# Kernel tuning notes

Measured on AMD Instinct MI355X. Metric: run time of the kernel, lower is better.

The kernel has to match this reference:

```python
import jax, jax.numpy as jnp
import numpy as np

B, S, D, H = 4, 2048, 1024, 16
HD = D // H

def setup_inputs() -> dict:
    key = jax.random.key(0)
    ks = jax.random.split(key, 11)
    scale = 1.0 / np.sqrt(D)
    return {
        "query": jax.random.normal(ks[0], (B, S, D), jnp.float32),
        "key_": jax.random.normal(ks[1], (B, S, D), jnp.float32),
        "value": jax.random.normal(ks[2], (B, S, D), jnp.float32),
        "wq": jax.random.normal(ks[3], (D, D), jnp.float32) * scale,
        "bq": jnp.zeros((D,), jnp.float32),
        "wk": jax.random.normal(ks[4], (D, D), jnp.float32) * scale,
        "bk": jnp.zeros((D,), jnp.float32),
        "wv": jax.random.normal(ks[5], (D, D), jnp.float32) * scale,
        "bv": jnp.zeros((D,), jnp.float32),
        "wo": jax.random.normal(ks[6], (D, D), jnp.float32) * scale,
        "bo": jnp.zeros((D,), jnp.float32),
    }

def _split_heads(x):
    b, s, _ = x.shape
    return x.reshape(b, s, H, HD).transpose(0, 2, 1, 3)  # [B,H,S,HD]

def reference(query, key_, value, wq, bq, wk, bk, wv, bv, wo, bo):
    q = _split_heads(query @ wq + bq)
    k = _split_heads(key_ @ wk + bk)
    v = _split_heads(value @ wv + bv)
    scores = jnp.einsum('bhqd,bhkd->bhqk', q, k) / jnp.sqrt(jnp.float32(HD))
    attn = jax.nn.softmax(scores, axis=-1)
    ctx = jnp.einsum('bhqk,bhkd->bhqd', attn, v)
    ctx = ctx.transpose(0, 2, 1, 3).reshape(B, S, D)
    return ctx @ wo + bo
```

## Files before the change

### kernel.cpp

```cpp
#include <hip/hip_runtime.h>

typedef _Float16 f16;
typedef _Float16 f16x8 __attribute__((ext_vector_type(8)));
typedef _Float16 f16x4 __attribute__((ext_vector_type(4)));
typedef float    f32x4 __attribute__((ext_vector_type(4)));
typedef float    f32x16 __attribute__((ext_vector_type(16)));

#define MROWS 8192
#define KDIM  1024
#define SEQ   2048
#define HDIM  64
#define QKV_LD 3072

#if __has_builtin(__builtin_amdgcn_exp2f)
#define EXP2(x) __builtin_amdgcn_exp2f(x)
#else
#define EXP2(x) exp2f(x)
#endif

#define AS1 __attribute__((address_space(1)))
#define AS3 __attribute__((address_space(3)))

__device__ __forceinline__ int swz5(int row) { return (row ^ (row >> 3)) & 7; }

__global__ __launch_bounds__(256) void prep_k(const float* __restrict__ q_,
                                              const float* __restrict__ k_,
                                              const float* __restrict__ v_,
                                              const float* __restrict__ w0,
                                              const float* __restrict__ w1,
                                              const float* __restrict__ w2,
                                              const float* __restrict__ w3,
                                              const float* __restrict__ bq,
                                              const float* __restrict__ bk,
                                              const float* __restrict__ bv,
                                              f16* __restrict__ X16,
                                              f16* __restrict__ qkvT,
                                              f16* __restrict__ woT,
                                              float* __restrict__ b3) {
  __shared__ float t[32][33];
  const int bid = blockIdx.x;
  const int tid = threadIdx.x;
  if (bid < 24576) {
    int y = bid >> 13;
    int i = (bid & 8191) * 256 + tid;
    const float* src = (y == 0) ? q_ : (y == 1) ? k_ : v_;
    float4 v = ((const float4*)src)[i];
    f16x4 o = { (f16)v.x, (f16)v.y, (f16)v.z, (f16)v.w };
    *(f16x4*)&X16[(size_t)y * 8388608 + (size_t)i * 4] = o;
  } else if (bid < 28672) {
    int local = bid - 24576;
    int z  = local >> 10;
    int by = ((local >> 5) & 31) * 32;
    int bx = (local & 31) * 32;
    const float* w = (z == 0) ? w0 : (z == 1) ? w1 : (z == 2) ? w2 : w3;
    f16* wt = (z == 3) ? woT : (qkvT + z * 1048576);
    int tx = tid & 31, ty = tid >> 5;
    #pragma unroll
    for (int i = ty; i < 32; i += 8) t[i][tx] = w[(size_t)(by + i) * KDIM + bx + tx];
    __syncthreads();
    #pragma unroll
    for (int i = ty; i < 32; i += 8) wt[(size_t)(bx + i) * KDIM + by + tx] = (f16)t[tx][i];
  } else {
    int i = (bid - 28672) * 256 + tid;
    float v;
    if (i < 1024) v = bq[i]; else if (i < 2048) v = bk[i - 1024]; else v = bv[i - 2048];
    b3[i] = v;
  }
}

template<bool OUT_F16>
__global__ __launch_bounds__(256) void gemm_k(const f16* __restrict__ A0, size_t aStride,
                                              const f16* __restrict__ Bt,
                                              const float* __restrict__ bias,
                                              void* __restrict__ Cout, int ldc) {
  __shared__ f16 sA[128 * 64];
  __shared__ f16 sB[128 * 64];
  const int tid  = threadIdx.x;
  const int lane = tid & 63;
  const int r    = lane & 15;
  const int q    = lane >> 4;
  const int wave = tid >> 6;
  const int m0 = blockIdx.x * 128;
  const int ng = blockIdx.z * 1024 + blockIdx.y * 128;
  const int wm = (wave >> 1) * 64;
  const int wn = (wave & 1) * 64;
  const f16* A = A0 + (size_t)blockIdx.z * aStride;

  f32x4 acc[4][4];
  #pragma unroll
  for (int i = 0; i < 4; ++i)
    #pragma unroll
    for (int j = 0; j < 4; ++j) acc[i][j] = (f32x4){0.f, 0.f, 0.f, 0.f};

  for (int kt = 0; kt < KDIM; kt += 64) {
    #pragma unroll
    for (int issue = 0; issue < 4; ++issue) {
      int g   = issue * 256 + tid;
      int row = g >> 3;
      int csw = (g & 7) ^ (row & 7);
      const f16* gA = A  + (size_t)(m0 + row) * KDIM + kt + csw * 8;
      const f16* gB = Bt + (size_t)(ng + row) * KDIM + kt + csw * 8;
      int lb = __builtin_amdgcn_readfirstlane((issue * 256 + (tid & ~63)) * 16);
      __builtin_amdgcn_global_load_lds((const AS1 void*)gA,
                                       (AS3 void*)((char*)sA + lb), 16, 0, 0);
      __builtin_amdgcn_global_load_lds((const AS1 void*)gB,
                                       (AS3 void*)((char*)sB + lb), 16, 0, 0);
    }
    __syncthreads();
    #pragma unroll
    for (int kk = 0; kk < 64; kk += 32) {
      f16x8 af[4], bf[4];
      #pragma unroll
      for (int mi = 0; mi < 4; ++mi) {
        int row = wm + mi * 16 + r;
        int cs  = ((kk >> 3) + q) ^ (row & 7);
        af[mi] = *(const f16x8*)&sA[row * 64 + cs * 8];
      }
      #pragma unroll
      for (int ni = 0; ni < 4; ++ni) {
        int row = wn + ni * 16 + r;
        int cs  = ((kk >> 3) + q) ^ (row & 7);
        bf[ni] = *(const f16x8*)&sB[row * 64 + cs * 8];
      }
      #pragma unroll
      for (int mi = 0; mi < 4; ++mi)
        #pragma unroll
        for (int ni = 0; ni < 4; ++ni)
          acc[mi][ni] = __builtin_amdgcn_mfma_f32_16x16x32_f16(af[mi], bf[ni], acc[mi][ni], 0, 0, 0);
    }
    __syncthreads();
  }
  #pragma unroll
  for (int ni = 0; ni < 4; ++ni) {
    int col = ng + wn + ni * 16 + r;
    float bv = bias[col];
    #pragma unroll
    for (int mi = 0; mi < 4; ++mi) {
      int rowb = m0 + wm + mi * 16 + q * 4;
      #pragma unroll
      for (int reg = 0; reg < 4; ++reg) {
        float v = acc[mi][ni][reg] + bv;
        if constexpr (OUT_F16) ((f16*)Cout)[(size_t)(rowb + reg) * ldc + col] = (f16)v;
        else                   ((float*)Cout)[(size_t)(rowb + reg) * ldc + col] = v;
      }
    }
  }
}

__global__ __launch_bounds__(512, 2) void gemm256_k(const f16* __restrict__ A0,
                                                    const f16* __restrict__ Bt,
                                                    const float* __restrict__ bias,
                                                    f16* __restrict__ Cout) {
  __shared__ f16 smem[65536];
  const int tid  = threadIdx.x;
  const int lane = tid & 63;
  const int r    = lane & 15;
  const int q    = lane >> 4;
  const int wave = tid >> 6;
  const int wm   = wave >> 2;
  const int wn   = wave & 3;

  const int id  = blockIdx.x;
  const int swz = (id & 7) * 48 + (id >> 3);
  const int bx  = swz & 31;
  const int by  = swz >> 5;
  const int m0  = bx * 256;
  const int n0  = by * 256;
  const f16* A  = A0 + (size_t)(by >> 2) * 8388608;

  const int srow0 = tid >> 3;
  const int srow1 = (512 + tid) >> 3;
  const int sg0 = (tid & 7) ^ (srow0 & 7);
  const int sg1 = (tid & 7) ^ (srow1 & 7);
  const f16* gA0 = A  + (size_t)(m0 + srow0) * KDIM + sg0 * 8;
  const f16* gA1 = A  + (size_t)(m0 + srow1) * KDIM + sg1 * 8;
  const f16* gB0 = Bt + (size_t)(n0 + srow0) * KDIM + sg0 * 8;
  const f16* gB1 = Bt + (size_t)(n0 + srow1) * KDIM + sg1 * 8;
  const int lb0 = __builtin_amdgcn_readfirstlane((tid & ~63) * 16);
  const int lb1 = __builtin_amdgcn_readfirstlane((512 + (tid & ~63)) * 16);

  auto issueA = [&](int s, int hi) {
    char* base = (char*)smem + (s & 1) * 65536 + hi * 16384;
    const f16* s0 = gA0 + (size_t)hi * (128 * KDIM) + s * 64;
    const f16* s1 = gA1 + (size_t)hi * (128 * KDIM) + s * 64;
    __builtin_amdgcn_global_load_lds((const AS1 void*)s0, (AS3 void*)(base + lb0), 16, 0, 0);
    __builtin_amdgcn_global_load_lds((const AS1 void*)s1, (AS3 void*)(base + lb1), 16, 0, 0);
  };
  auto issueB = [&](int s, int hi) {
    char* base = (char*)smem + (s & 1) * 65536 + 32768 + hi * 16384;
    const f16* s0 = gB0 + (size_t)hi * (128 * KDIM) + s * 64;
    const f16* s1 = gB1 + (size_t)hi * (128 * KDIM) + s * 64;
    __builtin_amdgcn_global_load_lds((const AS1 void*)s0, (AS3 void*)(base + lb0), 16, 0, 0);
    __builtin_amdgcn_global_load_lds((const AS1 void*)s1, (AS3 void*)(base + lb1), 16, 0, 0);
  };

  auto readA = [&](int s, int qa, f16x8 (&af)[4][2]) {
    const f16* rg = smem + (s & 1) * 32768 + qa * 8192;
    #pragma unroll
    for (int mi = 0; mi < 4; ++mi) {
      int rl = wm * 64 + mi * 16 + r;
      #pragma unroll
      for (int kk2 = 0; kk2 < 2; ++kk2) {
        int g = kk2 * 4 + q;
        af[mi][kk2] = *(const f16x8*)&rg[rl * 64 + ((g ^ (rl & 7)) * 8)];
      }
    }
  };
  auto readB = [&](int s, int qb, f16x8 (&bf)[2][2]) {
    const f16* rg = smem + (s & 1) * 32768 + 16384 + qb * 8192;
    #pragma unroll
    for (int ni = 0; ni < 2; ++ni) {
      int rl = wn * 32 + ni * 16 + r;
      #pragma unroll
      for (int kk2 = 0; kk2 < 2; ++kk2) {
        int g = kk2 * 4 + q;
        bf[ni][kk2] = *(const f16x8*)&rg[rl * 64 + ((g ^ (rl & 7)) * 8)];
      }
    }
  };

  f32x4 acc[8][4];
  #pragma unroll
  for (int i = 0; i < 8; ++i)
    #pragma unroll
    for (int j = 0; j < 4; ++j) acc[i][j] = (f32x4){0.f, 0.f, 0.f, 0.f};

  auto mmaQ = [&](f16x8 (&af)[4][2], f16x8 (&bf)[2][2], int qa, int qb) {
    __builtin_amdgcn_s_setprio(1);
    #pragma unroll
    for (int kk2 = 0; kk2 < 2; ++kk2)
      #pragma unroll
      for (int mi = 0; mi < 4; ++mi)
        #pragma unroll
        for (int ni = 0; ni < 2; ++ni)
          acc[qa * 4 + mi][qb * 2 + ni] =
            __builtin_amdgcn_mfma_f32_16x16x32_f16(af[mi][kk2], bf[ni][kk2],
                                                   acc[qa * 4 + mi][qb * 2 + ni], 0, 0, 0);
    __builtin_amdgcn_s_setprio(0);
  };

  auto bar = [] {
    __builtin_amdgcn_sched_barrier(0);
    __builtin_amdgcn_s_barrier();
    __builtin_amdgcn_sched_barrier(0);
  };

  issueA(0, 0); issueB(0, 0); issueB(0, 1); issueA(0, 1);
  issueB(1, 0); issueA(1, 0); issueB(1, 1);
  asm volatile("s_waitcnt vmcnt(6)");
  bar();

  f16x8 alo[4][2], ahi[4][2], blo[2][2], bhi[2][2];
  #pragma unroll 1
  for (int s = 0; s < 16; ++s) {
    readA(s, 0, alo);
    readB(s, 0, blo);
    if (s + 1 < 16) issueA(s + 1, 1);
    bar();
    mmaQ(alo, blo, 0, 0);
    bar();
    readB(s, 1, bhi);
    if (s + 2 < 16) issueB(s + 2, 0);
    bar();
    mmaQ(alo, bhi, 0, 1);
    bar();
    readA(s, 1, ahi);
    if (s + 2 < 16) issueA(s + 2, 0);
    bar();
    mmaQ(ahi, bhi, 1, 1);
    bar();
    if (s + 2 < 16) issueB(s + 2, 1);
    if (s < 14)       { asm volatile("s_waitcnt vmcnt(6)"); }
    else if (s == 14) { asm volatile("s_waitcnt vmcnt(0)"); }
    bar();
    mmaQ(ahi, blo, 1, 0);
    bar();
  }

  if (by >= 8) {
    #pragma unroll
    for (int mi8 = 0; mi8 < 8; ++mi8) {
      int rowb = m0 + (mi8 >> 2) * 128 + wm * 64 + (mi8 & 3) * 16 + q * 4;
      int bb = rowb >> 11, ss = rowb & 2047;
      #pragma unroll
      for (int ni4 = 0; ni4 < 4; ++ni4) {
        int col = n0 + (ni4 >> 1) * 128 + wn * 32 + (ni4 & 1) * 16 + r;
        int vcol = col - 2048;
        float bv = bias[col];
        f16x4 o = { (f16)(acc[mi8][ni4][0] + bv), (f16)(acc[mi8][ni4][1] + bv),
                    (f16)(acc[mi8][ni4][2] + bv), (f16)(acc[mi8][ni4][3] + bv) };
        size_t row2 = (size_t)bb * 2048 + 2 * vcol + (ss >> 10);
        *(f16x4*)&Cout[row2 * QKV_LD + 2048 + (ss & 1023)] = o;
      }
    }
  } else {
    #pragma unroll
    for (int mi8 = 0; mi8 < 8; ++mi8) {
      int rowb = m0 + (mi8 >> 2) * 128 + wm * 64 + (mi8 & 3) * 16 + q * 4;
      #pragma unroll
      for (int ni4 = 0; ni4 < 4; ++ni4) {
        int col = n0 + (ni4 >> 1) * 128 + wn * 32 + (ni4 & 1) * 16 + r;
        float bv = bias[col];
        #pragma unroll
        for (int reg = 0; reg < 4; ++reg)
          Cout[(size_t)(rowb + reg) * QKV_LD + col] = (f16)(acc[mi8][ni4][reg] + bv);
      }
    }
  }
}

__global__ __launch_bounds__(512) void attn_k(const f16* __restrict__ qkv,
                                              f16* __restrict__ ctx) {
  __shared__ f16 smem[16384];
  const int tid  = threadIdx.x;
  const int lane = tid & 63;
  const int wave = tid >> 6;
  const int n    = lane & 31;
  const int q32  = lane >> 5;
  const int flat = blockIdx.x + (blockIdx.y << 3) + (blockIdx.z << 7);
  const int qt = flat >> 6;
  const int hb = flat & 63;
  const int h  = hb & 15;
  const int b  = hb >> 4;

  const f16* Qb  = qkv + (size_t)b * SEQ * QKV_LD + h * HDIM;
  const int qrow = qt * 256 + wave * 32 + n;

  f16x8 qf[4];
  {
    const f16* qp = Qb + (size_t)qrow * QKV_LD + q32 * 8;
    const f16 sc = (f16)(0.125f * 1.44269504f);
    #pragma unroll
    for (int cc = 0; cc < 4; ++cc) qf[cc] = *(const f16x8*)(qp + cc * 16) * sc;
  }

  const int r0 = tid >> 3, c0 = tid & 7;
  const f16* gK0 = Qb + 1024 + (size_t)r0 * QKV_LD + (c0 ^ swz5(r0)) * 8;
  const f16* VtB = qkv + ((size_t)b * 2048 + 2 * (h * HDIM + r0)) * QKV_LD + 2048
                   + (c0 ^ swz5(r0)) * 8;
  const int lb = __builtin_amdgcn_readfirstlane((tid & ~63) * 16);

  int vt_t = 0;
  auto stage = [&](int bufbyte) {
    char* base = (char*)smem + bufbyte + lb;
    const f16* gV = VtB + (size_t)(vt_t >> 4) * QKV_LD + (vt_t & 15) * 64;
    __builtin_amdgcn_global_load_lds((const AS1 void*)gK0, (AS3 void*)(base), 16, 0, 0);
    __builtin_amdgcn_global_load_lds((const AS1 void*)gV, (AS3 void*)(base + 8192), 16, 0, 0);
    gK0 += 64 * QKV_LD; ++vt_t;
  };

  f32x16 ot[2];
  #pragma unroll
  for (int db = 0; db < 2; ++db)
    #pragma unroll
    for (int i = 0; i < 16; ++i) ot[db][i] = 0.f;
  float ls = 0.f;

  auto compute = [&](int bufe) {
    const f16* sK = smem + bufe;
    const f16* sV = smem + bufe + 4096;
    f16x4 p[2][4];
    #pragma unroll
    for (int kc = 0; kc < 2; ++kc) {
      f32x16 st;
      #pragma unroll
      for (int i = 0; i < 16; ++i) st[i] = -2.8853901817f;
      __builtin_amdgcn_s_setprio(1);
      #pragma unroll
      for (int cc = 0; cc < 4; ++cc) {
        int row = kc * 32 + n;
        f16x8 kf = *(const f16x8*)&sK[row * 64 + (((cc * 2 + q32) ^ swz5(row)) * 8)];
        st = __builtin_amdgcn_mfma_f32_32x32x16_f16(kf, qf[cc], st, 0, 0, 0);
      }
      __builtin_amdgcn_s_setprio(0);
      #pragma unroll
      for (int g = 0; g < 4; ++g) {
        float e0 = EXP2(st[4 * g + 0]);
        float e1 = EXP2(st[4 * g + 1]);
        float e2 = EXP2(st[4 * g + 2]);
        float e3 = EXP2(st[4 * g + 3]);
        ls += (e0 + e1) + (e2 + e3);
        p[kc][g] = (f16x4){ (f16)e0, (f16)e1, (f16)e2, (f16)e3 };
      }
    }
    __builtin_amdgcn_s_setprio(1);
    #pragma unroll
    for (int db = 0; db < 2; ++db) {
      int row = db * 32 + n;
      int fr = swz5(row);
      const f16* vrow = &sV[row * 64];
      #pragma unroll
      for (int cc = 0; cc < 4; ++cc) {
        int hg = (2 * cc) ^ fr;
        f16x4 vlo = *(const f16x4*)&vrow[hg * 8 + q32 * 4];
        f16x4 vhi = *(const f16x4*)&vrow[(hg ^ 1) * 8 + q32 * 4];
        f16x8 vf = __builtin_shufflevector(vlo, vhi, 0, 1, 2, 3, 4, 5, 6, 7);
        f16x8 pf = __builtin_shufflevector(p[cc >> 1][2 * (cc & 1)],
                                           p[cc >> 1][2 * (cc & 1) + 1],
                                           0, 1, 2, 3, 4, 5, 6, 7);
        ot[db] = __builtin_amdgcn_mfma_f32_32x32x16_f16(vf, pf, ot[db], 0, 0, 0);
      }
    }
    __builtin_amdgcn_s_setprio(0);
  };

  stage(0);
  #pragma unroll 1
  for (int it = 0; it < 32; it += 2) {
    __syncthreads();
    stage(16384);
    compute(0);
    __syncthreads();
    if (it + 2 < 32) stage(0);
    compute(8192);
  }

  ls += __shfl_xor(ls, 32);
  float inv = 1.0f / ls;

  __syncthreads();
  f16* sO = smem;
  int nl = wave * 32 + n;
  int fo = swz5(nl);
  #pragma unroll
  for (int db = 0; db < 2; ++db)
    #pragma unroll
    for (int g = 0; g < 4; ++g) {
      f16x4 o = { (f16)(ot[db][4 * g + 0] * inv), (f16)(ot[db][4 * g + 1] * inv),
                  (f16)(ot[db][4 * g + 2] * inv), (f16)(ot[db][4 * g + 3] * inv) };
      *(f16x4*)&sO[nl * 64 + (((db * 4 + g) ^ fo) * 8) + q32 * 4] = o;
    }
  __syncthreads();
  #pragma unroll
  for (int issue = 0; issue < 4; ++issue) {
    int g = issue * 512 + tid;
    int rr = g >> 3, sg = g & 7;
    f16x8 v = *(const f16x8*)&sO[rr * 64 + ((sg ^ swz5(rr)) * 8)];
    *(f16x8*)&ctx[(size_t)(b * SEQ + qt * 256 + rr) * KDIM + h * HDIM + sg * 8] = v;
  }
}

extern "C" void kernel_launch(void* const* d_in, const int* in_sizes, int n_in,
                              void* d_out, int out_size, void* d_ws, size_t ws_size,
                              hipStream_t stream) {
  (void)in_sizes; (void)n_in; (void)out_size; (void)ws_size;
  const float* query = (const float*)d_in[0];
  const float* key_  = (const float*)d_in[1];
  const float* value = (const float*)d_in[2];
  const float* wq = (const float*)d_in[3];
  const float* bq = (const float*)d_in[4];
  const float* wk = (const float*)d_in[5];
  const float* bk = (const float*)d_in[6];
  const float* wv = (const float*)d_in[7];
  const float* bv = (const float*)d_in[8];
  const float* wo = (const float*)d_in[9];
  const float* bo = (const float*)d_in[10];
  float* out = (float*)d_out;

  char* ws = (char*)d_ws;
  f16*   X16  = (f16*)(ws);
  f16*   qkvT = (f16*)(ws + 50331648);
  f16*   woT  = (f16*)(ws + 56623104);
  float* b3   = (float*)(ws + 58720256);
  f16*   QKV  = (f16*)(ws + 58736640);
  f16*   ctx  = (f16*)(ws);

  prep_k<<<dim3(28684), 256, 0, stream>>>(query, key_, value, wq, wk, wv, wo,
                                          bq, bk, bv, X16, qkvT, woT, b3);

  gemm256_k<<<dim3(384), 512, 0, stream>>>(X16, qkvT, b3, QKV);
  attn_k<<<dim3(8, 16, 4), 512, 0, stream>>>(QKV, ctx);
  gemm_k<false><<<dim3(64, 8, 1), 256, 0, stream>>>(ctx, (size_t)0, woT, bo, (void*)out, 1024);
}
```

Before: 335.8 us.

## Software-pipeline QK^T of next tile with softmax and PV of current tile

After: 384.5 us. 1.14x slower.

```diff
diff --git a/kernel.cpp b/kernel.cpp
--- a/kernel.cpp
+++ b/kernel.cpp
@@ -311,7 +311,7 @@
 
 __global__ __launch_bounds__(512) void attn_k(const f16* __restrict__ qkv,
                                               f16* __restrict__ ctx) {
-  __shared__ f16 smem[16384];
+  __shared__ f16 smem[32768];
   const int tid  = threadIdx.x;
   const int lane = tid & 63;
   const int wave = tid >> 6;
@@ -356,33 +356,34 @@
     for (int i = 0; i < 16; ++i) ot[db][i] = 0.f;
   float ls = 0.f;
 
-  auto compute = [&](int bufe) {
+  auto qkh = [&](int bufe, int kc, f32x16& st) {
     const f16* sK = smem + bufe;
+    #pragma unroll
+    for (int i = 0; i < 16; ++i) st[i] = -2.8853901817f;
+    int row = kc * 32 + n;
+    __builtin_amdgcn_s_setprio(1);
+    #pragma unroll
+    for (int cc = 0; cc < 4; ++cc) {
+      f16x8 kf = *(const f16x8*)&sK[row * 64 + (((cc * 2 + q32) ^ swz5(row)) * 8)];
+      st = __builtin_amdgcn_mfma_f32_32x32x16_f16(kf, qf[cc], st, 0, 0, 0);
+    }
+    __builtin_amdgcn_s_setprio(0);
+  };
+
+  auto exph = [&](f32x16& st, f16x4* pg) {
+    #pragma unroll
+    for (int g = 0; g < 4; ++g) {
+      float e0 = EXP2(st[4 * g + 0]);
+      float e1 = EXP2(st[4 * g + 1]);
+      float e2 = EXP2(st[4 * g + 2]);
+      float e3 = EXP2(st[4 * g + 3]);
+      ls += (e0 + e1) + (e2 + e3);
+      pg[g] = (f16x4){ (f16)e0, (f16)e1, (f16)e2, (f16)e3 };
+    }
+  };
+
+  auto pv = [&](f16x4 (&p)[2][4], int bufe) {
     const f16* sV = smem + bufe + 4096;
-    f16x4 p[2][4];
-    #pragma unroll
-    for (int kc = 0; kc < 2; ++kc) {
-      f32x16 st;
-      #pragma unroll
-      for (int i = 0; i < 16; ++i) st[i] = -2.8853901817f;
-      __builtin_amdgcn_s_setprio(1);
-      #pragma unroll
-      for (int cc = 0; cc < 4; ++cc) {
-        int row = kc * 32 + n;
-        f16x8 kf = *(const f16x8*)&sK[row * 64 + (((cc * 2 + q32) ^ swz5(row)) * 8)];
-        st = __builtin_amdgcn_mfma_f32_32x32x16_f16(kf, qf[cc], st, 0, 0, 0);
-      }
-      __builtin_amdgcn_s_setprio(0);
-      #pragma unroll
-      for (int g = 0; g < 4; ++g) {
-        float e0 = EXP2(st[4 * g + 0]);
-        float e1 = EXP2(st[4 * g + 1]);
-        float e2 = EXP2(st[4 * g + 2]);
-        float e3 = EXP2(st[4 * g + 3]);
-        ls += (e0 + e1) + (e2 + e3);
-        p[kc][g] = (f16x4){ (f16)e0, (f16)e1, (f16)e2, (f16)e3 };
-      }
-    }
     __builtin_amdgcn_s_setprio(1);
     #pragma unroll
     for (int db = 0; db < 2; ++db) {
@@ -404,15 +405,32 @@
     __builtin_amdgcn_s_setprio(0);
   };
 
+  auto body = [&](int curE, int nxtE, int stgB, int t,
+                  f32x16& c0, f32x16& c1, f32x16& n0v, f32x16& n1v) {
+    __syncthreads();
+    if (t + 2 < 32) stage(stgB);
+    f16x4 p[2][4];
+    if (t + 1 < 32) qkh(nxtE, 0, n0v);
+    exph(c0, p[0]);
+    if (t + 1 < 32) qkh(nxtE, 1, n1v);
+    exph(c1, p[1]);
+    pv(p, curE);
+  };
+
   stage(0);
+  stage(16384);
+  __syncthreads();
+  f32x16 sA0, sA1, sB0, sB1;
+  qkh(0, 0, sA0);
+  qkh(0, 1, sA1);
+
   #pragma unroll 1
-  for (int it = 0; it < 32; it += 2) {
-    __syncthreads();
-    stage(16384);
-    compute(0);
-    __syncthreads();
-    if (it + 2 < 32) stage(0);
-    compute(8192);
+  for (int k = 0; k < 8; ++k) {
+    int t0 = k * 4;
+    body(0,     8192,  32768, t0 + 0, sA0, sA1, sB0, sB1);
+    body(8192,  16384, 49152, t0 + 1, sB0, sB1, sA0, sA1);
+    body(16384, 24576, 0,     t0 + 2, sA0, sA1, sB0, sB1);
+    body(24576, 0,     16384, t0 + 3, sB0, sB1, sA0, sA1);
   }
 
   ls += __shfl_xor(ls, 32);
```
